# Kernel tuning notes

Measured on AMD Instinct MI355X. Metric: run time of the kernel, lower is better.

The kernel has to match this reference:

```python
import jax, jax.numpy as jnp
import numpy as np

N_SENT = 65536
N_PAIRS = 8192
D = 690          # 3 * cnn_filters (cnn_filters = 230)
CLASS_NUM = 53


def setup_inputs() -> dict:
    key = jax.random.key(0)
    k1, k2 = jax.random.split(key)
    rng = np.random.default_rng(0)
    # Every pair id appears at least once so the number of non-empty bags is
    # statically N_PAIRS (TF drops empty bins dynamically; we avoid that).
    extra = rng.integers(0, N_PAIRS, N_SENT - N_PAIRS)
    epid_np = np.concatenate([np.arange(N_PAIRS), extra])
    rng.shuffle(epid_np)
    counts_np = np.bincount(epid_np, minlength=N_PAIRS)
    max_count = int(counts_np.max())  # static padded bag width
    inputs = jax.random.normal(k1, (N_SENT, D), dtype=jnp.float32)
    emb_table = jax.random.normal(k2, (CLASS_NUM, D), dtype=jnp.float32) * 0.02
    # labels are consistent within a bag (distant supervision): label per pair id
    pair_labels = rng.integers(0, CLASS_NUM, N_PAIRS)
    labels_np = pair_labels[epid_np]
    return {
        "inputs": inputs,
        "emb_table": emb_table,
        "labels": jnp.asarray(labels_np, dtype=jnp.int64),
        "entity_pair_id": jnp.asarray(epid_np, dtype=jnp.int64),
        "num_pairs": N_PAIRS,
        "max_count": max_count,
    }


def reference(inputs, emb_table, labels, entity_pair_id, num_pairs, max_count):
    # 1) sort sentences by entity_pair_id descending (tf.nn.top_k over full len)
    order = jnp.argsort(-entity_pair_id, stable=True)
    labels_s = labels[order]
    sen = inputs[order]                                   # [N, D]
    epid_s = entity_pair_id[order]
    # 2) per-bag counts, in descending-pair-id order (bincount then reverse)
    counts = jnp.bincount(epid_s.astype(jnp.int32), length=num_pairs)[::-1]  # [P]
    ends = jnp.cumsum(counts)                             # [P]
    starts = ends - counts
    bag_labels = labels_s[ends - 1]                       # [P] one label per bag
    # 3) ragged-to-padded index matrix + mask (sparse-tensor trick in TF)
    pos = jnp.arange(max_count)
    mask = pos[None, :] < counts[:, None]                 # [P, M] bool
    idx = jnp.where(mask, starts[:, None] + pos[None, :], 0)
    sen_m = sen[idx]                                      # [P, M, D]
    # 4) selective attention: score each sentence against its relation embedding
    rel = emb_table[bag_labels]                           # [P, D]
    score = jnp.einsum('pmd,pd->pm', sen_m, rel)          # [P, M]
    w = jnp.exp(score - jnp.max(score, axis=-1, keepdims=True))
    w = w * mask.astype(sen.dtype)
    alpha = w / (jnp.sum(w, axis=-1, keepdims=True) + 1e-8)
    sen_att = jnp.einsum('pm,pmd->pd', alpha, sen_m)      # [P, D]
    return sen_att, bag_labels
```

## Files before the change

### kernel.cpp

```cpp
#include <hip/hip_runtime.h>
#include <math.h>

#define MAXC 64
#define BLK  256
#define DD   690
#define NF2  345
#define NJ   6

__global__ void sa_scatter_kernel(const int* __restrict__ epid, int n_sent,
                                  int* __restrict__ counts, int* __restrict__ idxmat) {
    int i = blockIdx.x * blockDim.x + threadIdx.x;
    if (i >= n_sent) return;
    int q = epid[i];
    int r = atomicAdd(&counts[q], 1);
    if (r < MAXC) idxmat[(q << 6) + r] = i;
}

__global__ __launch_bounds__(BLK, 4)
void sa_bag_wave_kernel(const float* __restrict__ inputs,
                        const float* __restrict__ emb,
                        const int* __restrict__ labels,
                        const int* __restrict__ counts,
                        const int* __restrict__ idxmat,
                        float* __restrict__ out_att,
                        float* __restrict__ out_lab,
                        int P) {
    const int lane = threadIdx.x & 63;
    const int wid  = threadIdx.x >> 6;
    const int p = (blockIdx.x << 2) + wid;
    if (p >= P) return;
    const int q = P - 1 - p;
    int cnt = counts[q];
    if (cnt > MAXC) cnt = MAXC;
    const int* bag = idxmat + (q << 6);
    int myidx = (lane < cnt) ? bag[lane] : 0;

    const int idx0 = __shfl(myidx, 0);
    const int lab  = labels[idx0];

    const float2* rel2 = (const float2*)(emb + (size_t)lab * DD);
    float2 rel_r[NJ];
    #pragma unroll
    for (int j = 0; j < NJ; ++j) {
        int f = lane + 64 * j;
        rel_r[j] = (f < NF2) ? rel2[f] : make_float2(0.f, 0.f);
    }

    float2 acc[NJ];
    #pragma unroll
    for (int j = 0; j < NJ; ++j) acc[j] = make_float2(0.f, 0.f);
    float sw = 0.f;

    float2 a0[NJ], a1[NJ], b0[NJ], b1[NJ];

    auto load_pair = [&](float2* r0, float2* r1, int base) {
        int i0 = __shfl(myidx, base);
        int i1 = __shfl(myidx, (base + 1) & 63);
        const float2* row0 = (const float2*)(inputs + (size_t)i0 * DD);
        const float2* row1 = (const float2*)(inputs + (size_t)i1 * DD);
        #pragma unroll
        for (int j = 0; j < NJ; ++j) {
            int f = lane + 64 * j;
            r0[j] = (f < NF2) ? row0[f] : make_float2(0.f, 0.f);
            r1[j] = (f < NF2) ? row1[f] : make_float2(0.f, 0.f);
        }
    };

    auto process_pair = [&](const float2* r0, const float2* r1, int base) {
        float s0 = 0.f, s1 = 0.f;
        #pragma unroll
        for (int j = 0; j < NJ; ++j) {
            s0 = fmaf(r0[j].x, rel_r[j].x, s0);
            s0 = fmaf(r0[j].y, rel_r[j].y, s0);
            s1 = fmaf(r1[j].x, rel_r[j].x, s1);
            s1 = fmaf(r1[j].y, rel_r[j].y, s1);
        }
        #pragma unroll
        for (int off = 32; off; off >>= 1) {
            s0 += __shfl_xor(s0, off);
            s1 += __shfl_xor(s1, off);
        }
        float w0 = __expf(s0);
        float w1 = (base + 1 < cnt) ? __expf(s1) : 0.f;
        sw += w0 + w1;
        #pragma unroll
        for (int j = 0; j < NJ; ++j) {
            acc[j].x = fmaf(w0, r0[j].x, acc[j].x);
            acc[j].x = fmaf(w1, r1[j].x, acc[j].x);
            acc[j].y = fmaf(w0, r0[j].y, acc[j].y);
            acc[j].y = fmaf(w1, r1[j].y, acc[j].y);
        }
    };

    const int npair = (cnt + 1) >> 1;
    load_pair(a0, a1, 0);
    for (int m = 0; m < npair; m += 2) {
        if (m + 1 < npair) load_pair(b0, b1, 2 * (m + 1));
        process_pair(a0, a1, 2 * m);
        if (m + 1 < npair) {
            if (m + 2 < npair) load_pair(a0, a1, 2 * (m + 2));
            process_pair(b0, b1, 2 * (m + 1));
        }
    }

    const float inv = 1.0f / (sw + 1e-8f);
    float2* out2 = (float2*)(out_att + (size_t)p * DD);
    #pragma unroll
    for (int j = 0; j < NJ; ++j) {
        int f = lane + 64 * j;
        if (f < NF2) out2[f] = make_float2(acc[j].x * inv, acc[j].y * inv);
    }
    if (lane == 0) out_lab[p] = (float)lab;
}

extern "C" void kernel_launch(void* const* d_in, const int* in_sizes, int n_in,
                              void* d_out, int out_size, void* d_ws, size_t ws_size,
                              hipStream_t stream) {
    const float* inputs = (const float*)d_in[0];
    const float* emb    = (const float*)d_in[1];
    const int*   labels = (const int*)d_in[2];
    const int*   epid   = (const int*)d_in[3];

    const int n_sent = in_sizes[2];
    const int P      = out_size / (DD + 1);

    int* counts = (int*)d_ws;
    int* idxmat = counts + P;

    hipMemsetAsync(counts, 0, (size_t)P * sizeof(int), stream);
    sa_scatter_kernel<<<(n_sent + BLK - 1) / BLK, BLK, 0, stream>>>(epid, n_sent, counts, idxmat);

    float* out_att = (float*)d_out;
    float* out_lab = out_att + (size_t)P * DD;
    const int nblk = (P + 3) / 4;
    sa_bag_wave_kernel<<<nblk, BLK, 0, stream>>>(inputs, emb, labels, counts, idxmat,
                                                 out_att, out_lab, P);
}
```

Before: 48.01 us.

## Use persistent atomic-ticket bag scheduling and precompute bag labels in scatter

The bag kernel becomes persistent: a fixed grid of 1024 blocks, where each wavefront repeatedly claims the next bag index through a global atomic ticket. This is meant to balance the uneven per-bag work. The scatter kernel now writes each bag's label into slot 63 of its index row and writes the output label directly, so the bag kernel skips the dependent label gather. MAXC is cut to 56 to free that slot, which silently drops sentences if any bag holds more than 56. The ticket also adds one atomic per bag.

```diff
diff --git a/kernel.cpp b/kernel.cpp
--- a/kernel.cpp
+++ b/kernel.cpp
@@ -1,116 +1,125 @@
 #include <hip/hip_runtime.h>
 #include <math.h>
 
-#define MAXC 64
+#define MAXC 56
 #define BLK  256
 #define DD   690
 #define NF2  345
 #define NJ   6
 
-__global__ void sa_scatter_kernel(const int* __restrict__ epid, int n_sent,
-                                  int* __restrict__ counts, int* __restrict__ idxmat) {
+__global__ void sa_scatter_kernel(const int* __restrict__ epid,
+                                  const int* __restrict__ labels, int n_sent,
+                                  int* __restrict__ counts, int* __restrict__ idxmat,
+                                  float* __restrict__ out_lab, int P) {
     int i = blockIdx.x * blockDim.x + threadIdx.x;
     if (i >= n_sent) return;
     int q = epid[i];
     int r = atomicAdd(&counts[q], 1);
     if (r < MAXC) idxmat[(q << 6) + r] = i;
+    if (r == 0) {
+        int lab = labels[i];
+        idxmat[(q << 6) + 63] = lab;
+        out_lab[P - 1 - q] = (float)lab;
+    }
 }
 
 __global__ __launch_bounds__(BLK, 4)
 void sa_bag_wave_kernel(const float* __restrict__ inputs,
                         const float* __restrict__ emb,
-                        const int* __restrict__ labels,
                         const int* __restrict__ counts,
                         const int* __restrict__ idxmat,
+                        int* __restrict__ ticket,
                         float* __restrict__ out_att,
-                        float* __restrict__ out_lab,
                         int P) {
     const int lane = threadIdx.x & 63;
-    const int wid  = threadIdx.x >> 6;
-    const int p = (blockIdx.x << 2) + wid;
-    if (p >= P) return;
-    const int q = P - 1 - p;
-    int cnt = counts[q];
-    if (cnt > MAXC) cnt = MAXC;
-    const int* bag = idxmat + (q << 6);
-    int myidx = (lane < cnt) ? bag[lane] : 0;
 
-    const int idx0 = __shfl(myidx, 0);
-    const int lab  = labels[idx0];
+    for (;;) {
+        int t;
+        if (lane == 0) t = atomicAdd(ticket, 1);
+        t = __shfl(t, 0);
+        if (t >= P) return;
 
-    const float2* rel2 = (const float2*)(emb + (size_t)lab * DD);
-    float2 rel_r[NJ];
-    #pragma unroll
-    for (int j = 0; j < NJ; ++j) {
-        int f = lane + 64 * j;
-        rel_r[j] = (f < NF2) ? rel2[f] : make_float2(0.f, 0.f);
-    }
+        const int p = t;
+        const int q = P - 1 - p;
+        int cnt = counts[q];
+        if (cnt > MAXC) cnt = MAXC;
+        const int* bag = idxmat + (q << 6);
+        int myidx = (lane < cnt) ? bag[lane] : 0;
+        const int lab = bag[63];
 
-    float2 acc[NJ];
-    #pragma unroll
-    for (int j = 0; j < NJ; ++j) acc[j] = make_float2(0.f, 0.f);
-    float sw = 0.f;
-
-    float2 a0[NJ], a1[NJ], b0[NJ], b1[NJ];
-
-    auto load_pair = [&](float2* r0, float2* r1, int base) {
-        int i0 = __shfl(myidx, base);
-        int i1 = __shfl(myidx, (base + 1) & 63);
-        const float2* row0 = (const float2*)(inputs + (size_t)i0 * DD);
-        const float2* row1 = (const float2*)(inputs + (size_t)i1 * DD);
+        const float2* rel2 = (const float2*)(emb + (size_t)lab * DD);
+        float2 rel_r[NJ];
         #pragma unroll
         for (int j = 0; j < NJ; ++j) {
             int f = lane + 64 * j;
-            r0[j] = (f < NF2) ? row0[f] : make_float2(0.f, 0.f);
-            r1[j] = (f < NF2) ? row1[f] : make_float2(0.f, 0.f);
+            rel_r[j] = (f < NF2) ? rel2[f] : make_float2(0.f, 0.f);
         }
-    };
 
-    auto process_pair = [&](const float2* r0, const float2* r1, int base) {
-        float s0 = 0.f, s1 = 0.f;
+        float2 acc[NJ];
+        #pragma unroll
+        for (int j = 0; j < NJ; ++j) acc[j] = make_float2(0.f, 0.f);
+        float sw = 0.f;
+
+        float2 a0[NJ], a1[NJ], b0[NJ], b1[NJ];
+
+        auto load_pair = [&](float2* r0, float2* r1, int base) {
+            int i0 = __shfl(myidx, base);
+            int i1 = __shfl(myidx, (base + 1) & 63);
+            const float2* row0 = (const float2*)(inputs + (size_t)i0 * DD);
+            const float2* row1 = (const float2*)(inputs + (size_t)i1 * DD);
+            #pragma unroll
+            for (int j = 0; j < NJ; ++j) {
+                int f = lane + 64 * j;
+                r0[j] = (f < NF2) ? row0[f] : make_float2(0.f, 0.f);
+                r1[j] = (f < NF2) ? row1[f] : make_float2(0.f, 0.f);
+            }
+        };
+
+        auto process_pair = [&](const float2* r0, const float2* r1, int base) {
+            float s0 = 0.f, s1 = 0.f;
+            #pragma unroll
+            for (int j = 0; j < NJ; ++j) {
+                s0 = fmaf(r0[j].x, rel_r[j].x, s0);
+                s0 = fmaf(r0[j].y, rel_r[j].y, s0);
+                s1 = fmaf(r1[j].x, rel_r[j].x, s1);
+                s1 = fmaf(r1[j].y, rel_r[j].y, s1);
+            }
+            #pragma unroll
+            for (int off = 32; off; off >>= 1) {
+                s0 += __shfl_xor(s0, off);
+                s1 += __shfl_xor(s1, off);
+            }
+            float w0 = __expf(s0);
+            float w1 = (base + 1 < cnt) ? __expf(s1) : 0.f;
+            sw += w0 + w1;
+            #pragma unroll
+            for (int j = 0; j < NJ; ++j) {
+                acc[j].x = fmaf(w0, r0[j].x, acc[j].x);
+                acc[j].x = fmaf(w1, r1[j].x, acc[j].x);
+                acc[j].y = fmaf(w0, r0[j].y, acc[j].y);
+                acc[j].y = fmaf(w1, r1[j].y, acc[j].y);
+            }
+        };
+
+        const int npair = (cnt + 1) >> 1;
+        load_pair(a0, a1, 0);
+        for (int m = 0; m < npair; m += 2) {
+            if (m + 1 < npair) load_pair(b0, b1, 2 * (m + 1));
+            process_pair(a0, a1, 2 * m);
+            if (m + 1 < npair) {
+                if (m + 2 < npair) load_pair(a0, a1, 2 * (m + 2));
+                process_pair(b0, b1, 2 * (m + 1));
+            }
+        }
+
+        const float inv = 1.0f / (sw + 1e-8f);
+        float2* out2 = (float2*)(out_att + (size_t)p * DD);
         #pragma unroll
         for (int j = 0; j < NJ; ++j) {
-            s0 = fmaf(r0[j].x, rel_r[j].x, s0);
-            s0 = fmaf(r0[j].y, rel_r[j].y, s0);
-            s1 = fmaf(r1[j].x, rel_r[j].x, s1);
-            s1 = fmaf(r1[j].y, rel_r[j].y, s1);
-        }
-        #pragma unroll
-        for (int off = 32; off; off >>= 1) {
-            s0 += __shfl_xor(s0, off);
-            s1 += __shfl_xor(s1, off);
-        }
-        float w0 = __expf(s0);
-        float w1 = (base + 1 < cnt) ? __expf(s1) : 0.f;
-        sw += w0 + w1;
-        #pragma unroll
-        for (int j = 0; j < NJ; ++j) {
-            acc[j].x = fmaf(w0, r0[j].x, acc[j].x);
-            acc[j].x = fmaf(w1, r1[j].x, acc[j].x);
-            acc[j].y = fmaf(w0, r0[j].y, acc[j].y);
-            acc[j].y = fmaf(w1, r1[j].y, acc[j].y);
-        }
-    };
-
-    const int npair = (cnt + 1) >> 1;
-    load_pair(a0, a1, 0);
-    for (int m = 0; m < npair; m += 2) {
-        if (m + 1 < npair) load_pair(b0, b1, 2 * (m + 1));
-        process_pair(a0, a1, 2 * m);
-        if (m + 1 < npair) {
-            if (m + 2 < npair) load_pair(a0, a1, 2 * (m + 2));
-            process_pair(b0, b1, 2 * (m + 1));
+            int f = lane + 64 * j;
+            if (f < NF2) out2[f] = make_float2(acc[j].x * inv, acc[j].y * inv);
         }
     }
-
-    const float inv = 1.0f / (sw + 1e-8f);
-    float2* out2 = (float2*)(out_att + (size_t)p * DD);
-    #pragma unroll
-    for (int j = 0; j < NJ; ++j) {
-        int f = lane + 64 * j;
-        if (f < NF2) out2[f] = make_float2(acc[j].x * inv, acc[j].y * inv);
-    }
-    if (lane == 0) out_lab[p] = (float)lab;
 }
 
 extern "C" void kernel_launch(void* const* d_in, const int* in_sizes, int n_in,
@@ -125,14 +134,17 @@
     const int P      = out_size / (DD + 1);
 
     int* counts = (int*)d_ws;
-    int* idxmat = counts + P;
-
-    hipMemsetAsync(counts, 0, (size_t)P * sizeof(int), stream);
-    sa_scatter_kernel<<<(n_sent + BLK - 1) / BLK, BLK, 0, stream>>>(epid, n_sent, counts, idxmat);
+    int* ticket = counts + P;
+    int* idxmat = ticket + 1;
 
     float* out_att = (float*)d_out;
     float* out_lab = out_att + (size_t)P * DD;
-    const int nblk = (P + 3) / 4;
-    sa_bag_wave_kernel<<<nblk, BLK, 0, stream>>>(inputs, emb, labels, counts, idxmat,
-                                                 out_att, out_lab, P);
+
+    hipMemsetAsync(counts, 0, (size_t)(P + 1) * sizeof(int), stream);
+    sa_scatter_kernel<<<(n_sent + BLK - 1) / BLK, BLK, 0, stream>>>(
+        epid, labels, n_sent, counts, idxmat, out_lab, P);
+
+    const int nblk = 1024;
+    sa_bag_wave_kernel<<<nblk, BLK, 0, stream>>>(inputs, emb, counts, idxmat,
+                                                 ticket, out_att, P);
 }
```

Measured after the change: 163.2 us. 240% more time.
